# Performance work log

Hardware: AMD Instinct MI355X
Metric: run time of the kernel (lower is better)

The kernel has to match this reference:

```python
import jax, jax.numpy as jnp
import numpy as np

INPUT_SIZE = 2
HIDDEN_SIZE = 5
OUTPUT_SIZE = 1
SEQ_LEN = 512
BATCH = 8192


def setup_inputs() -> dict:
    key = jax.random.key(0)
    ks = jax.random.split(key, 7)
    H, I = HIDDEN_SIZE, INPUT_SIZE
    bound = 1.0 / np.sqrt(H)  # PyTorch nn.LSTM / nn.Linear init range
    x = jax.random.normal(ks[0], (SEQ_LEN, BATCH, I), dtype=jnp.float32)
    W_ih = jax.random.uniform(ks[1], (4 * H, I), minval=-bound, maxval=bound, dtype=jnp.float32)
    W_hh = jax.random.uniform(ks[2], (4 * H, H), minval=-bound, maxval=bound, dtype=jnp.float32)
    b_ih = jax.random.uniform(ks[3], (4 * H,), minval=-bound, maxval=bound, dtype=jnp.float32)
    b_hh = jax.random.uniform(ks[4], (4 * H,), minval=-bound, maxval=bound, dtype=jnp.float32)
    W_lin = jax.random.uniform(ks[5], (OUTPUT_SIZE, H), minval=-bound, maxval=bound, dtype=jnp.float32)
    b_lin = jax.random.uniform(ks[6], (OUTPUT_SIZE,), minval=-bound, maxval=bound, dtype=jnp.float32)
    return {"x": x, "W_ih": W_ih, "W_hh": W_hh, "b_ih": b_ih, "b_hh": b_hh,
            "W_lin": W_lin, "b_lin": b_lin}


def _lstm_last_hidden(x, W_ih, W_hh, b_ih, b_hh):
    # x: [S, B, I]. Precompute the input projection as one big GEMM,
    # then scan the recurrence. PyTorch gate order: i, f, g, o.
    S, B, _ = x.shape
    H = W_hh.shape[1]
    x_proj = jnp.einsum('sbi,gi->sbg', x, W_ih) + b_ih + b_hh  # [S, B, 4H]

    def step(carry, xp):
        h, c = carry
        gates = xp + h @ W_hh.T  # [B, 4H]
        i, f, g, o = jnp.split(gates, 4, axis=-1)
        i = jax.nn.sigmoid(i)
        f = jax.nn.sigmoid(f)
        g = jnp.tanh(g)
        o = jax.nn.sigmoid(o)
        c = f * c + i * g
        h = o * jnp.tanh(c)
        return (h, c), None

    h0 = jnp.zeros((B, H), dtype=x.dtype)
    c0 = jnp.zeros((B, H), dtype=x.dtype)
    (h_last, _), _ = jax.lax.scan(step, (h0, c0), x_proj)
    return h_last  # [B, H]


def reference(x, W_ih, W_hh, b_ih, b_hh, W_lin, b_lin):
    # Original applies the linear to all timesteps then takes the last row;
    # mathematically identical (and cheaper) to project only the last hidden state.
    h_last = _lstm_last_hidden(x, W_ih, W_hh, b_ih, b_hh)
    return h_last @ W_lin.T + b_lin  # [B, OUTPUT_SIZE]
```

## Files before the change

kernel.cpp:

```cpp
#include <hip/hip_runtime.h>

constexpr int S = 512, B = 8192, H = 5;
constexpr float KN1 = -1.44269504088896340736f;
constexpr float KN2 = 2.0f * KN1;

__device__ __forceinline__ float fexp2(float x) { return __builtin_amdgcn_exp2f(x); }
__device__ __forceinline__ float frcp(float x)  { return __builtin_amdgcn_rcpf(x); }

#define SWZ(v, imm) __int_as_float(__builtin_amdgcn_ds_swizzle(__float_as_int(v), (imm)))
#define ROR8(v) __int_as_float(__builtin_amdgcn_mov_dpp(__float_as_int(v), 0x128, 0xF, 0xF, false))

__global__ __launch_bounds__(256, 2) void lstm_kernel(
    const float* __restrict__ x,
    const float* __restrict__ W_ih,
    const float* __restrict__ W_hh,
    const float* __restrict__ b_ih,
    const float* __restrict__ b_hh,
    const float* __restrict__ W_lin,
    const float* __restrict__ b_lin,
    float* __restrict__ out)
{
  const int tid   = blockIdx.x * blockDim.x + threadIdx.x;
  const int chain = tid >> 4;
  const int l     = tid & 15;
  const int u     = l >> 3;
  const int j     = l & 7;
  const int jm    = (j < H) ? j : H - 1;

  const int r1 = (u ? H : 0) + jm;
  const int r2 = (u ? 3 * H : 2 * H) + jm;
  const float s2 = u ? KN1 : KN2;
  const float eA = u ? 1.0f : 2.0f;
  const float eB = u ? 0.0f : -1.0f;

  float w1x0 = W_ih[r1 * 2 + 0] * KN1, w1x1 = W_ih[r1 * 2 + 1] * KN1;
  float w2x0 = W_ih[r2 * 2 + 0] * s2,  w2x1 = W_ih[r2 * 2 + 1] * s2;
  float w1h[H], w2h[H];
  #pragma unroll
  for (int k = 0; k < H; ++k) {
    w1h[k] = W_hh[r1 * H + k] * KN1;
    w2h[k] = W_hh[r2 * H + k] * s2;
  }
  const float b1 = (b_ih[r1] + b_hh[r1]) * KN1;
  const float b2 = (b_ih[r2] + b_hh[r2]) * s2;

  float h = 0.0f, c = 0.0f;
  float hg[H] = {0, 0, 0, 0, 0};

  const float2* __restrict__ x2 = (const float2*)x;

  auto step = [&](float2 xv) {
    float a1 = fmaf(xv.x, w1x0, b1);
    a1 = fmaf(xv.y, w1x1, a1);
    float a2 = fmaf(xv.x, w2x0, b2);
    a2 = fmaf(xv.y, w2x1, a2);
    #pragma unroll
    for (int k = 0; k < H; ++k) {
      a1 = fmaf(hg[k], w1h[k], a1);
      a2 = fmaf(hg[k], w2h[k], a2);
    }
    const float v1 = frcp(1.0f + fexp2(a1));
    const float r2v = frcp(1.0f + fexp2(a2));
    const float go = fmaf(r2v, eA, eB);
    const float p  = v1 * go;
    const float pr = ROR8(p);
    c = fmaf(v1, c, pr);
    const float th = fmaf(2.0f, frcp(1.0f + fexp2(c * KN2)), -1.0f);
    h = go * th;
    hg[0] = SWZ(h, 0x110);
    hg[1] = SWZ(h, 0x130);
    hg[2] = SWZ(h, 0x150);
    hg[3] = SWZ(h, 0x170);
    hg[4] = SWZ(h, 0x190);
  };

  constexpr int CH = 4;
  float2 buf0[CH], buf1[CH];
  #pragma unroll
  for (int t = 0; t < CH; ++t) buf0[t] = x2[(size_t)t * B + chain];

  for (int t0 = 0; t0 < S; t0 += 2 * CH) {
    #pragma unroll
    for (int t = 0; t < CH; ++t) buf1[t] = x2[(size_t)(t0 + CH + t) * B + chain];
    #pragma unroll
    for (int t = 0; t < CH; ++t) step(buf0[t]);
    if (t0 + 2 * CH < S) {
      #pragma unroll
      for (int t = 0; t < CH; ++t) buf0[t] = x2[(size_t)(t0 + 2 * CH + t) * B + chain];
    }
    #pragma unroll
    for (int t = 0; t < CH; ++t) step(buf1[t]);
  }

  float p = (u == 1 && j < H) ? h * W_lin[jm] : 0.0f;
  p += SWZ(p, 0x41F);
  p += SWZ(p, 0x81F);
  p += SWZ(p, 0x101F);
  if ((tid & 15) == 8) out[chain] = p + b_lin[0];
}

extern "C" void kernel_launch(void* const* d_in, const int* in_sizes, int n_in,
                              void* d_out, int out_size, void* d_ws, size_t ws_size,
                              hipStream_t stream) {
  const float* x     = (const float*)d_in[0];
  const float* W_ih  = (const float*)d_in[1];
  const float* W_hh  = (const float*)d_in[2];
  const float* b_ih  = (const float*)d_in[3];
  const float* b_hh  = (const float*)d_in[4];
  const float* W_lin = (const float*)d_in[5];
  const float* b_lin = (const float*)d_in[6];
  float* out = (float*)d_out;

  const int threads = B * 16;
  dim3 grid(threads / 256), block(256);
  hipLaunchKernelGGL(lstm_kernel, grid, block, 0, stream,
                     x, W_ih, W_hh, b_ih, b_hh, W_lin, b_lin, out);
}
```

Before: 81.54 us.

## Pack two LSTM chains per 16-lane group with packed FP32 FMAs

Each 16-lane group now processes two batch chains instead of one, halving the thread count. The gate pre-activations are computed as 2-wide vectors so the compiler can emit packed FMA instructions, the tanh(c) evaluation is shared across the two chains by lane half, and x is read as float4. The aim is to raise useful work per instruction and cut idle lanes on this latency-bound recurrence. In exchange, each thread holds more registers and a longer serial dependency chain per step, and fewer waves are available to hide latency, with launch bounds relaxed to one block per SIMD.

```diff
diff --git a/kernel.cpp b/kernel.cpp
--- a/kernel.cpp
+++ b/kernel.cpp
@@ -1,4 +1,6 @@
 #include <hip/hip_runtime.h>
+
+typedef float v2f __attribute__((ext_vector_type(2)));
 
 constexpr int S = 512, B = 8192, H = 5;
 constexpr float KN1 = -1.44269504088896340736f;
@@ -10,7 +12,7 @@
 #define SWZ(v, imm) __int_as_float(__builtin_amdgcn_ds_swizzle(__float_as_int(v), (imm)))
 #define ROR8(v) __int_as_float(__builtin_amdgcn_mov_dpp(__float_as_int(v), 0x128, 0xF, 0xF, false))
 
-__global__ __launch_bounds__(256, 2) void lstm_kernel(
+__global__ __launch_bounds__(256, 1) void lstm_kernel(
     const float* __restrict__ x,
     const float* __restrict__ W_ih,
     const float* __restrict__ W_hh,
@@ -20,83 +22,99 @@
     const float* __restrict__ b_lin,
     float* __restrict__ out)
 {
-  const int tid   = blockIdx.x * blockDim.x + threadIdx.x;
-  const int chain = tid >> 4;
-  const int l     = tid & 15;
-  const int u     = l >> 3;
-  const int j     = l & 7;
-  const int jm    = (j < H) ? j : H - 1;
+  const int tid = blockIdx.x * blockDim.x + threadIdx.x;
+  const int grp = tid >> 4;
+  const int cA  = 2 * grp, cB = 2 * grp + 1;
+  const int l   = tid & 15;
+  const int u   = l >> 3;
+  const int j   = l & 7;
+  const int jm  = (j < H) ? j : H - 1;
 
-  const int r1 = (u ? H : 0) + jm;
-  const int r2 = (u ? 3 * H : 2 * H) + jm;
-  const float s2 = u ? KN1 : KN2;
-  const float eA = u ? 1.0f : 2.0f;
-  const float eB = u ? 0.0f : -1.0f;
+  const int r1A = (u ? H : 0) + jm;
+  const int r2A = (u ? 3 * H : 2 * H) + jm;
+  const int r1B = (u ? 0 : H) + jm;
+  const int r2B = (u ? 2 * H : 3 * H) + jm;
+  const float s2A = u ? KN1 : KN2;
+  const float s2B = u ? KN2 : KN1;
+  const float eAA = u ? 1.f : 2.f, eBA = u ? 0.f : -1.f;
+  const float eAB = u ? 2.f : 1.f, eBB = u ? -1.f : 0.f;
 
-  float w1x0 = W_ih[r1 * 2 + 0] * KN1, w1x1 = W_ih[r1 * 2 + 1] * KN1;
-  float w2x0 = W_ih[r2 * 2 + 0] * s2,  w2x1 = W_ih[r2 * 2 + 1] * s2;
-  float w1h[H], w2h[H];
+  v2f wx0A = {W_ih[r1A * 2 + 0] * KN1, W_ih[r2A * 2 + 0] * s2A};
+  v2f wx1A = {W_ih[r1A * 2 + 1] * KN1, W_ih[r2A * 2 + 1] * s2A};
+  v2f wx0B = {W_ih[r1B * 2 + 0] * KN1, W_ih[r2B * 2 + 0] * s2B};
+  v2f wx1B = {W_ih[r1B * 2 + 1] * KN1, W_ih[r2B * 2 + 1] * s2B};
+  v2f whA[H], whB[H];
   #pragma unroll
   for (int k = 0; k < H; ++k) {
-    w1h[k] = W_hh[r1 * H + k] * KN1;
-    w2h[k] = W_hh[r2 * H + k] * s2;
+    whA[k] = (v2f){W_hh[r1A * H + k] * KN1, W_hh[r2A * H + k] * s2A};
+    whB[k] = (v2f){W_hh[r1B * H + k] * KN1, W_hh[r2B * H + k] * s2B};
   }
-  const float b1 = (b_ih[r1] + b_hh[r1]) * KN1;
-  const float b2 = (b_ih[r2] + b_hh[r2]) * s2;
+  const v2f bA = {(b_ih[r1A] + b_hh[r1A]) * KN1, (b_ih[r2A] + b_hh[r2A]) * s2A};
+  const v2f bB = {(b_ih[r1B] + b_hh[r1B]) * KN1, (b_ih[r2B] + b_hh[r2B]) * s2B};
 
-  float h = 0.0f, c = 0.0f;
-  float hg[H] = {0, 0, 0, 0, 0};
+  float hA = 0.f, cAr = 0.f, hB = 0.f, cBr = 0.f;
+  float hgA[H] = {0, 0, 0, 0, 0}, hgB[H] = {0, 0, 0, 0, 0};
 
-  const float2* __restrict__ x2 = (const float2*)x;
+  const float4* __restrict__ x4 = (const float4*)x;
 
-  auto step = [&](float2 xv) {
-    float a1 = fmaf(xv.x, w1x0, b1);
-    a1 = fmaf(xv.y, w1x1, a1);
-    float a2 = fmaf(xv.x, w2x0, b2);
-    a2 = fmaf(xv.y, w2x1, a2);
+  auto step = [&](float4 xv) {
+    v2f aA = bA, aB = bB;
+    aA = __builtin_elementwise_fma((v2f){xv.x, xv.x}, wx0A, aA);
+    aB = __builtin_elementwise_fma((v2f){xv.z, xv.z}, wx0B, aB);
+    aA = __builtin_elementwise_fma((v2f){xv.y, xv.y}, wx1A, aA);
+    aB = __builtin_elementwise_fma((v2f){xv.w, xv.w}, wx1B, aB);
     #pragma unroll
     for (int k = 0; k < H; ++k) {
-      a1 = fmaf(hg[k], w1h[k], a1);
-      a2 = fmaf(hg[k], w2h[k], a2);
+      aA = __builtin_elementwise_fma((v2f){hgA[k], hgA[k]}, whA[k], aA);
+      aB = __builtin_elementwise_fma((v2f){hgB[k], hgB[k]}, whB[k], aB);
     }
-    const float v1 = frcp(1.0f + fexp2(a1));
-    const float r2v = frcp(1.0f + fexp2(a2));
-    const float go = fmaf(r2v, eA, eB);
-    const float p  = v1 * go;
-    const float pr = ROR8(p);
-    c = fmaf(v1, c, pr);
-    const float th = fmaf(2.0f, frcp(1.0f + fexp2(c * KN2)), -1.0f);
-    h = go * th;
-    hg[0] = SWZ(h, 0x110);
-    hg[1] = SWZ(h, 0x130);
-    hg[2] = SWZ(h, 0x150);
-    hg[3] = SWZ(h, 0x170);
-    hg[4] = SWZ(h, 0x190);
+    const float e1A = fexp2(aA.x), e2A = fexp2(aA.y);
+    const float e1B = fexp2(aB.x), e2B = fexp2(aB.y);
+    const float v1A = frcp(1.f + e1A), r2A_ = frcp(1.f + e2A);
+    const float v1B = frcp(1.f + e1B), r2B_ = frcp(1.f + e2B);
+    const float goA = fmaf(r2A_, eAA, eBA);
+    const float goB = fmaf(r2B_, eAB, eBB);
+    const float pA = v1A * goA;
+    const float pB = v1B * goB;
+    const float prA = ROR8(pA);
+    const float prB = ROR8(pB);
+    cAr = fmaf(v1A, cAr, prA);
+    cBr = fmaf(v1B, cBr, prB);
+    const float cM = u ? cAr : cBr;
+    const float th = fmaf(2.f, frcp(1.f + fexp2(cM * KN2)), -1.f);
+    hA = goA * th;
+    hB = goB * th;
+    hgA[0] = SWZ(hA, 0x110); hgB[0] = SWZ(hB, 0x010);
+    hgA[1] = SWZ(hA, 0x130); hgB[1] = SWZ(hB, 0x030);
+    hgA[2] = SWZ(hA, 0x150); hgB[2] = SWZ(hB, 0x050);
+    hgA[3] = SWZ(hA, 0x170); hgB[3] = SWZ(hB, 0x070);
+    hgA[4] = SWZ(hA, 0x190); hgB[4] = SWZ(hB, 0x090);
   };
 
   constexpr int CH = 4;
-  float2 buf0[CH], buf1[CH];
+  float4 buf0[CH], buf1[CH];
   #pragma unroll
-  for (int t = 0; t < CH; ++t) buf0[t] = x2[(size_t)t * B + chain];
+  for (int t = 0; t < CH; ++t) buf0[t] = x4[(size_t)t * (B / 2) + grp];
 
   for (int t0 = 0; t0 < S; t0 += 2 * CH) {
     #pragma unroll
-    for (int t = 0; t < CH; ++t) buf1[t] = x2[(size_t)(t0 + CH + t) * B + chain];
+    for (int t = 0; t < CH; ++t) buf1[t] = x4[(size_t)(t0 + CH + t) * (B / 2) + grp];
     #pragma unroll
     for (int t = 0; t < CH; ++t) step(buf0[t]);
     if (t0 + 2 * CH < S) {
       #pragma unroll
-      for (int t = 0; t < CH; ++t) buf0[t] = x2[(size_t)(t0 + 2 * CH + t) * B + chain];
+      for (int t = 0; t < CH; ++t) buf0[t] = x4[(size_t)(t0 + 2 * CH + t) * (B / 2) + grp];
     }
     #pragma unroll
     for (int t = 0; t < CH; ++t) step(buf1[t]);
   }
 
-  float p = (u == 1 && j < H) ? h * W_lin[jm] : 0.0f;
+  float p = 0.f;
+  if (j < H) p = (u ? hA : hB) * W_lin[jm];
   p += SWZ(p, 0x41F);
   p += SWZ(p, 0x81F);
   p += SWZ(p, 0x101F);
-  if ((tid & 15) == 8) out[chain] = p + b_lin[0];
+  if (j == 0) out[u ? cA : cB] = p + b_lin[0];
 }
 
 extern "C" void kernel_launch(void* const* d_in, const int* in_sizes, int n_in,
@@ -111,7 +129,7 @@
   const float* b_lin = (const float*)d_in[6];
   float* out = (float*)d_out;
 
-  const int threads = B * 16;
+  const int threads = (B / 2) * 16;
   dim3 grid(threads / 256), block(256);
   hipLaunchKernelGGL(lstm_kernel, grid, block, 0, stream,
                      x, W_ih, W_hh, b_ih, b_hh, W_lin, b_lin, out);
```

Result: slower. 88.54 us (+8.6%).

## Replace swizzle broadcasts with DPP row-rotate chain and packed FMA recurrence

Applied to the files above, without the earlier changes.

Instead of broadcasting the five hidden values through five ds_swizzle ops per step, each lane now rotates a single value through the 8-lane row with DPP row_ror:1, multiplying against pre-rotated weights (zero-padded for the three unused lanes). The two gate accumulators are packed into a 2-wide vector so the FMAs can map to packed FP32 instructions. The cell state is kept pre-scaled by -2*log2(e), which removes a multiply before the tanh exp, and the tanh/output-gate algebra is folded into a single FMA. This trades LDS-path swizzle latency on the serial recurrence for a dependent chain of eight DPP moves and more FMAs per step.

```diff
diff --git a/kernel.cpp b/kernel.cpp
--- a/kernel.cpp
+++ b/kernel.cpp
@@ -1,4 +1,6 @@
 #include <hip/hip_runtime.h>
+
+typedef float v2f __attribute__((ext_vector_type(2)));
 
 constexpr int S = 512, B = 8192, H = 5;
 constexpr float KN1 = -1.44269504088896340736f;
@@ -9,6 +11,7 @@
 
 #define SWZ(v, imm) __int_as_float(__builtin_amdgcn_ds_swizzle(__float_as_int(v), (imm)))
 #define ROR8(v) __int_as_float(__builtin_amdgcn_mov_dpp(__float_as_int(v), 0x128, 0xF, 0xF, false))
+#define ROR1(v) __int_as_float(__builtin_amdgcn_mov_dpp(__float_as_int(v), 0x121, 0xF, 0xF, false))
 
 __global__ __launch_bounds__(256, 2) void lstm_kernel(
     const float* __restrict__ x,
@@ -30,48 +33,51 @@
   const int r1 = (u ? H : 0) + jm;
   const int r2 = (u ? 3 * H : 2 * H) + jm;
   const float s2 = u ? KN1 : KN2;
-  const float eA = u ? 1.0f : 2.0f;
-  const float eB = u ? 0.0f : -1.0f;
+  const float eA = u ? 1.0f : 2.0f * KN2;
+  const float eB = u ? 0.0f : -KN2;
 
-  float w1x0 = W_ih[r1 * 2 + 0] * KN1, w1x1 = W_ih[r1 * 2 + 1] * KN1;
-  float w2x0 = W_ih[r2 * 2 + 0] * s2,  w2x1 = W_ih[r2 * 2 + 1] * s2;
-  float w1h[H], w2h[H];
+  v2f wx0 = {W_ih[r1 * 2 + 0] * KN1, W_ih[r2 * 2 + 0] * s2};
+  v2f wx1 = {W_ih[r1 * 2 + 1] * KN1, W_ih[r2 * 2 + 1] * s2};
+  v2f bb  = {(b_ih[r1] + b_hh[r1]) * KN1, (b_ih[r2] + b_hh[r2]) * s2};
+
+  v2f wrot[8];
   #pragma unroll
-  for (int k = 0; k < H; ++k) {
-    w1h[k] = W_hh[r1 * H + k] * KN1;
-    w2h[k] = W_hh[r2 * H + k] * s2;
+  for (int m = 0; m < 8; ++m) {
+    const int k = (j - m) & 7;
+    wrot[m] = (k < H) ? (v2f){W_hh[r1 * H + k] * KN1, W_hh[r2 * H + k] * s2}
+                      : (v2f){0.0f, 0.0f};
   }
-  const float b1 = (b_ih[r1] + b_hh[r1]) * KN1;
-  const float b2 = (b_ih[r2] + b_hh[r2]) * s2;
 
-  float h = 0.0f, c = 0.0f;
-  float hg[H] = {0, 0, 0, 0, 0};
+  float hsel = 0.0f;
+  float CS   = 0.0f;
+  float h    = 0.0f;
 
   const float2* __restrict__ x2 = (const float2*)x;
 
   auto step = [&](float2 xv) {
-    float a1 = fmaf(xv.x, w1x0, b1);
-    a1 = fmaf(xv.y, w1x1, a1);
-    float a2 = fmaf(xv.x, w2x0, b2);
-    a2 = fmaf(xv.y, w2x1, a2);
+    v2f a = bb;
+    a = __builtin_elementwise_fma((v2f){xv.x, xv.x}, wx0, a);
+    a = __builtin_elementwise_fma((v2f){xv.y, xv.y}, wx1, a);
+    float r = hsel;
     #pragma unroll
-    for (int k = 0; k < H; ++k) {
-      a1 = fmaf(hg[k], w1h[k], a1);
-      a2 = fmaf(hg[k], w2h[k], a2);
+    for (int m = 0; m < 8; ++m) {
+      a = __builtin_elementwise_fma((v2f){r, r}, wrot[m], a);
+      if (m < 7) r = ROR1(r);
     }
-    const float v1 = frcp(1.0f + fexp2(a1));
-    const float r2v = frcp(1.0f + fexp2(a2));
-    const float go = fmaf(r2v, eA, eB);
-    const float p  = v1 * go;
-    const float pr = ROR8(p);
-    c = fmaf(v1, c, pr);
-    const float th = fmaf(2.0f, frcp(1.0f + fexp2(c * KN2)), -1.0f);
-    h = go * th;
-    hg[0] = SWZ(h, 0x110);
-    hg[1] = SWZ(h, 0x130);
-    hg[2] = SWZ(h, 0x150);
-    hg[3] = SWZ(h, 0x170);
-    hg[4] = SWZ(h, 0x190);
+    const float e1  = fexp2(a.x);
+    const float e2  = fexp2(a.y);
+    const float v1  = frcp(1.0f + e1);
+    const float r2v = frcp(1.0f + e2);
+    const float gK  = fmaf(r2v, eA, eB);
+    const float p   = v1 * gK;
+    const float pr  = ROR8(p);
+    CS = fmaf(v1, CS, pr);
+    const float et = fexp2(CS);
+    const float rt = frcp(1.0f + et);
+    const float o2 = gK + gK;
+    h = fmaf(rt, o2, -gK);
+    const float hr = ROR8(h);
+    hsel = u ? h : hr;
   };
 
   constexpr int CH = 4;
@@ -92,11 +98,11 @@
     for (int t = 0; t < CH; ++t) step(buf1[t]);
   }
 
-  float p = (u == 1 && j < H) ? h * W_lin[jm] : 0.0f;
-  p += SWZ(p, 0x41F);
-  p += SWZ(p, 0x81F);
-  p += SWZ(p, 0x101F);
-  if ((tid & 15) == 8) out[chain] = p + b_lin[0];
+  float pv = (u == 1 && j < H) ? h * W_lin[jm] : 0.0f;
+  pv += SWZ(pv, 0x41F);
+  pv += SWZ(pv, 0x81F);
+  pv += SWZ(pv, 0x101F);
+  if ((tid & 15) == 8) out[chain] = pv + b_lin[0];
 }
 
 extern "C" void kernel_launch(void* const* d_in, const int* in_sizes, int n_in,
```

New measurement: 94.20 us. 15.5% more time.
